# Kernel optimization log

Measured on AMD Instinct MI355X. Metric: run time of the kernel, lower is better.

Reference implementation:

```python
import jax, jax.numpy as jnp
import numpy as np

N_NODES = 100000
N_EDGES = 640000
D_IN = 128
D_OUT = 128


def setup_inputs() -> dict:
    key = jax.random.key(0)
    k_x, k_w, k_v, k_r, k_c = jax.random.split(key, 5)
    x = jax.random.normal(k_x, (N_NODES, D_IN), dtype=jnp.float32)
    # Xavier-uniform init for weights, zeros for bias (matches module init)
    limit = float(np.sqrt(6.0 / (D_IN + D_OUT)))
    weights = jax.random.uniform(k_w, (D_IN, D_OUT), dtype=jnp.float32,
                                 minval=-limit, maxval=limit)
    bias = jnp.zeros((D_OUT,), dtype=jnp.float32)
    # Sparse normalized adjacency in COO form: value[e] * y[col[e]] scattered to row[e]
    edge_val = jax.random.uniform(k_v, (N_EDGES,), dtype=jnp.float32)
    row = jax.random.randint(k_r, (N_EDGES,), 0, N_NODES, dtype=jnp.int32)
    col = jax.random.randint(k_c, (N_EDGES,), 0, N_NODES, dtype=jnp.int32)
    return {"x": x, "weights": weights, "bias": bias,
            "edge_val": edge_val, "row": row, "col": col}


def reference(x, weights, bias, edge_val, row, col):
    # y = x @ W  (dense GEMM)  [N, D_OUT]
    y = x @ weights
    # SpMM: out[i] = sum_{e: row[e]==i} edge_val[e] * y[col[e]]
    msg = edge_val[:, None] * y[col]            # [E, D_OUT] irregular gather
    agg = jax.ops.segment_sum(msg, row, num_segments=x.shape[0])
    return agg + bias
```

## Files before the change

### kernel.cpp

```cpp
#include <hip/hip_runtime.h>
#include <hip/hip_bf16.h>


#define N_NODES 100000
#define N_EDGES 640000
#define D 128
#define ELL_K 16
#define OVF_CAP 8192
#define NB 391
#define BCAP 2048
#define CHUNK 2048
#define NCHUNKS 313
#define N_TILES 6250
#define ELL_P 17

typedef __attribute__((ext_vector_type(8))) short short8;
typedef __attribute__((ext_vector_type(4))) float f32x4;
typedef __attribute__((ext_vector_type(4))) ushort us4;

__device__ __forceinline__ ushort f2bf(float f) {
    uint u = __float_as_uint(f);
    u += 0x7fff + ((u >> 16) & 1);
    return (ushort)(u >> 16);
}
__device__ __forceinline__ float bflo(uint u) { return __uint_as_float(u << 16); }
__device__ __forceinline__ float bfhi(uint u) { return __uint_as_float(u & 0xffff0000u); }

__global__ __launch_bounds__(256, 4) void gemm_xw(const float* __restrict__ x,
                                                  const float* __restrict__ w,
                                                  ushort* __restrict__ y,
                                                  int* __restrict__ bucketCnt) {
    __shared__ ushort wt[128 * 128];
    const int tid = threadIdx.x;

    int gz = blockIdx.x * 256 + tid;
    if (gz <= NB) bucketCnt[gz] = 0;

    #pragma unroll
    for (int it = 0; it < 16; ++it) {
        int idx4 = tid + it * 256;
        int k = idx4 >> 5;
        int n0 = (idx4 & 31) * 4;
        float4 v = *(const float4*)(w + (size_t)idx4 * 4);
        float vv[4] = {v.x, v.y, v.z, v.w};
        #pragma unroll
        for (int q = 0; q < 4; ++q) {
            int n = n0 + q;
            wt[n * 128 + (k ^ ((n & 7) << 3))] = f2bf(vv[q]);
        }
    }
    __syncthreads();

    const int lane = tid & 63;
    const int l15 = lane & 15;
    const int h = lane >> 4;

    const int waveGlobal = blockIdx.x * 4 + (tid >> 6);
    const int nWaves = gridDim.x * 4;

    for (int t = waveGlobal; t < N_TILES; t += nWaves) {
        asm volatile("" ::: "memory");
        const float* xr = x + (size_t)(t * 16 + l15) * D;
        float4 xb[8];
        #pragma unroll
        for (int ks = 0; ks < 4; ++ks) {
            xb[2 * ks]     = *(const float4*)(xr + 32 * ks + 8 * h);
            xb[2 * ks + 1] = *(const float4*)(xr + 32 * ks + 8 * h + 4);
        }
        short8 a[4];
        #pragma unroll
        for (int ks = 0; ks < 4; ++ks) {
            const float* p0 = (const float*)&xb[2 * ks];
            const float* p1 = (const float*)&xb[2 * ks + 1];
            a[ks][0] = f2bf(p0[0]); a[ks][1] = f2bf(p0[1]);
            a[ks][2] = f2bf(p0[2]); a[ks][3] = f2bf(p0[3]);
            a[ks][4] = f2bf(p1[0]); a[ks][5] = f2bf(p1[1]);
            a[ks][6] = f2bf(p1[2]); a[ks][7] = f2bf(p1[3]);
        }
        f32x4 acc[8];
        #pragma unroll
        for (int j = 0; j < 8; ++j) acc[j] = (f32x4){0.f, 0.f, 0.f, 0.f};
        #pragma unroll
        for (int ks = 0; ks < 4; ++ks) {
            const int k0 = 32 * ks + 8 * h;
            #pragma unroll
            for (int j = 0; j < 8; ++j) {
                int n = 16 * j + l15;
                short8 b = *(const short8*)&wt[n * 128 + (k0 ^ ((n & 7) << 3))];
                acc[j] = __builtin_amdgcn_mfma_f32_16x16x32_bf16(b, a[ks], acc[j], 0, 0, 0);
            }
        }
        ushort* yn = y + (size_t)(t * 16 + l15) * D;
        #pragma unroll
        for (int j = 0; j < 8; ++j) {
            us4 o;
            o.x = f2bf(acc[j][0]); o.y = f2bf(acc[j][1]);
            o.z = f2bf(acc[j][2]); o.w = f2bf(acc[j][3]);
            *(us4*)(yn + 16 * j + 4 * h) = o;
        }
    }
}

__global__ __launch_bounds__(256) void partition_edges(const float* __restrict__ ev,
                                                       const int* __restrict__ row,
                                                       const int* __restrict__ col,
                                                       int* __restrict__ bucketCnt,
                                                       uint2* __restrict__ es0,
                                                       int* __restrict__ ovfCnt,
                                                       int* __restrict__ ovfRow,
                                                       int* __restrict__ ovfCol,
                                                       float* __restrict__ ovfVal) {
    __shared__ int hist[NB];
    __shared__ int cur[NB];
    const int tid = threadIdx.x;
    const int base = blockIdx.x * CHUNK;

    for (int t = tid; t < NB; t += 256) hist[t] = 0;
    __syncthreads();

    #pragma unroll
    for (int it = 0; it < CHUNK / 256; ++it) {
        int i = base + it * 256 + tid;
        if (i < N_EDGES) atomicAdd(&hist[row[i] >> 8], 1);
    }
    __syncthreads();

    for (int t = tid; t < NB; t += 256) {
        int h = hist[t];
        int start = (h > 0) ? atomicAdd(&bucketCnt[t], h) : 0;
        cur[t] = t * BCAP + start;
    }
    __syncthreads();

    #pragma unroll
    for (int it = 0; it < CHUNK / 256; ++it) {
        int i = base + it * 256 + tid;
        if (i < N_EDGES) {
            int r = row[i];
            int b = r >> 8;
            int p = atomicAdd(&cur[b], 1);
            if (p < (b + 1) * BCAP) {
                uint2 e;
                e.x = __float_as_uint(ev[i]);
                e.y = (uint)col[i] | ((uint)(r & 255) << 20);
                es0[p] = e;
            } else {
                int q = atomicAdd(ovfCnt, 1);
                if (q < OVF_CAP) {
                    ovfRow[q] = r;
                    ovfCol[q] = col[i];
                    ovfVal[q] = ev[i];
                }
            }
        }
    }
}

__global__ __launch_bounds__(256) void build_ell(const uint2* __restrict__ es0,
                                                 const int* __restrict__ bucketCnt,
                                                 float2* __restrict__ es,
                                                 int* __restrict__ ovfCnt,
                                                 int* __restrict__ ovfRow,
                                                 int* __restrict__ ovfCol,
                                                 float* __restrict__ ovfVal) {
    __shared__ float2 ell[256 * ELL_P];
    __shared__ int lcnt[256];
    const int tid = threadIdx.x;
    const int b = blockIdx.x;

    lcnt[tid] = 0;
    #pragma unroll
    for (int it = 0; it < ELL_P; ++it)
        ell[it * 256 + tid] = (float2){0.f, 0.f};
    __syncthreads();

    int cnt = bucketCnt[b];
    if (cnt > BCAP) cnt = BCAP;
    const uint2* src = es0 + (size_t)b * BCAP;

    for (int i = tid; i < cnt; i += 256) {
        uint2 e = src[i];
        int r = e.y >> 20;
        int p = atomicAdd(&lcnt[r], 1);
        if (p < ELL_K) {
            float2 rec;
            rec.x = __uint_as_float(e.x);
            rec.y = __uint_as_float(e.y & 0xFFFFFu);
            ell[r * ELL_P + p] = rec;
        } else {
            int q = atomicAdd(ovfCnt, 1);
            if (q < OVF_CAP) {
                ovfRow[q] = b * 256 + r;
                ovfCol[q] = (int)(e.y & 0xFFFFFu);
                ovfVal[q] = __uint_as_float(e.x);
            }
        }
    }
    __syncthreads();

    const int nbase = b * 256;
    int nvalid = N_NODES - nbase;
    if (nvalid > 256) nvalid = 256;

    float2* dst2 = es + (size_t)nbase * ELL_K;
    for (int t = tid; t < nvalid * ELL_K; t += 256) {
        int r = t >> 4, s = t & 15;
        dst2[t] = ell[r * ELL_P + s];
    }
}

__global__ __launch_bounds__(256) void spmm_ell(const ushort* __restrict__ y,
                                                const float2* __restrict__ es,
                                                const float* __restrict__ bias,
                                                float* __restrict__ out) {
    const int tid = threadIdx.x;
    const int c16 = tid & 15;
    const int n = blockIdx.x * 16 + (tid >> 4);

    const float4* er = (const float4*)(es + (size_t)n * ELL_K);
    float4 e0 = er[0], e1 = er[1], e2 = er[2], e3 = er[3];
    float4 e4 = er[4], e5 = er[5], e6 = er[6], e7 = er[7];

    const ushort* yb = y + c16 * 8;
    #define YLD(c) (*(const uint4*)(yb + ((size_t)__float_as_int(c) << 7)))
    uint4 u0 = YLD(e0.y), u1 = YLD(e0.w), u2 = YLD(e1.y), u3 = YLD(e1.w);
    uint4 u4 = YLD(e2.y), u5 = YLD(e2.w), u6 = YLD(e3.y), u7 = YLD(e3.w);
    uint4 u8 = YLD(e4.y), u9 = YLD(e4.w), uA = YLD(e5.y), uB = YLD(e5.w);
    uint4 uC = YLD(e6.y), uD = YLD(e6.w), uE = YLD(e7.y), uF = YLD(e7.w);
    #undef YLD

    float a[8] = {0.f, 0.f, 0.f, 0.f, 0.f, 0.f, 0.f, 0.f};
    #define FMA8(v, u) do { \
        a[0] += (v) * bflo((u).x); a[1] += (v) * bfhi((u).x); \
        a[2] += (v) * bflo((u).y); a[3] += (v) * bfhi((u).y); \
        a[4] += (v) * bflo((u).z); a[5] += (v) * bfhi((u).z); \
        a[6] += (v) * bflo((u).w); a[7] += (v) * bfhi((u).w); } while (0)
    FMA8(e0.x, u0); FMA8(e0.z, u1); FMA8(e1.x, u2); FMA8(e1.z, u3);
    FMA8(e2.x, u4); FMA8(e2.z, u5); FMA8(e3.x, u6); FMA8(e3.z, u7);
    FMA8(e4.x, u8); FMA8(e4.z, u9); FMA8(e5.x, uA); FMA8(e5.z, uB);
    FMA8(e6.x, uC); FMA8(e6.z, uD); FMA8(e7.x, uE); FMA8(e7.z, uF);
    #undef FMA8

    const float4 b0 = *(const float4*)(bias + c16 * 8);
    const float4 b1 = *(const float4*)(bias + c16 * 8 + 4);
    float4 o0 = {a[0] + b0.x, a[1] + b0.y, a[2] + b0.z, a[3] + b0.w};
    float4 o1 = {a[4] + b1.x, a[5] + b1.y, a[6] + b1.z, a[7] + b1.w};
    float* orow = out + ((size_t)n << 7) + c16 * 8;
    *(float4*)orow = o0;
    *(float4*)(orow + 4) = o1;
}

__global__ void ovf_fix(const ushort* __restrict__ y, const int* __restrict__ ovfRow,
                        const int* __restrict__ ovfCol, const float* __restrict__ ovfVal,
                        const int* __restrict__ ovfCnt, float* __restrict__ out) {
    int nOvf = *ovfCnt;
    if (nOvf > OVF_CAP) nOvf = OVF_CAP;
    int total = nOvf * 32;
    for (int idx = blockIdx.x * 256 + threadIdx.x; idx < total; idx += gridDim.x * 256) {
        int e = idx >> 5;
        int c = idx & 31;
        int r = ovfRow[e];
        int col = ovfCol[e];
        float v = ovfVal[e];
        uint2 u = *(const uint2*)(y + ((size_t)col << 7) + c * 4);
        atomicAdd(&out[(size_t)r * D + c * 4 + 0], v * bflo(u.x));
        atomicAdd(&out[(size_t)r * D + c * 4 + 1], v * bfhi(u.x));
        atomicAdd(&out[(size_t)r * D + c * 4 + 2], v * bflo(u.y));
        atomicAdd(&out[(size_t)r * D + c * 4 + 3], v * bfhi(u.y));
    }
}

extern "C" void kernel_launch(void* const* d_in, const int* in_sizes, int n_in,
                              void* d_out, int out_size, void* d_ws, size_t ws_size,
                              hipStream_t stream) {
    const float* x = (const float*)d_in[0];
    const float* w = (const float*)d_in[1];
    const float* bias = (const float*)d_in[2];
    const float* ev = (const float*)d_in[3];
    const int* row = (const int*)d_in[4];
    const int* col = (const int*)d_in[5];
    float* out = (float*)d_out;

    size_t off = 0;
    auto carve = [&](size_t bytes) -> void* {
        void* p = (char*)d_ws + off;
        off += (bytes + 255) & ~(size_t)255;
        return p;
    };
    ushort* y = (ushort*)carve((size_t)N_NODES * D * sizeof(ushort));
    float2* es = (float2*)carve((size_t)N_NODES * ELL_K * sizeof(float2));
    uint2* es0 = (uint2*)carve((size_t)NB * BCAP * sizeof(uint2));
    int* bucketCnt = (int*)carve((NB + 1) * sizeof(int));
    int* ovfCnt = bucketCnt + NB;
    int* ovfRow = (int*)carve(OVF_CAP * sizeof(int));
    int* ovfCol = (int*)carve(OVF_CAP * sizeof(int));
    float* ovfVal = (float*)carve(OVF_CAP * sizeof(float));

    gemm_xw<<<782, 256, 0, stream>>>(x, w, y, bucketCnt);
    partition_edges<<<NCHUNKS, 256, 0, stream>>>(ev, row, col, bucketCnt, es0,
                                                 ovfCnt, ovfRow, ovfCol, ovfVal);
    build_ell<<<NB, 256, 0, stream>>>(es0, bucketCnt, es,
                                      ovfCnt, ovfRow, ovfCol, ovfVal);
    spmm_ell<<<N_NODES / 16, 256, 0, stream>>>(y, es, bias, out);
    ovf_fix<<<16, 256, 0, stream>>>(y, ovfRow, ovfCol, ovfVal, ovfCnt, out);
}
```

Before: 88.21 us.

## Fuse ELL build with SpMM, register-cache W fragments, prefetch GEMM tiles

Merges build_ell, spmm_ell and ovf_fix into one kernel per 256-row bucket. The ELL slab stays in shared memory, so the global ELL buffer write and read-back go away. Overflow edges are handled per block through a small shared list followed by atomics, and bucket overflow (more than BCAP edges) is now silently dropped. The GEMM keeps all W fragments in registers, software-prefetches the next x tile, uses 512 blocks with launch bounds 2, and partition uses larger chunks. This cuts launch count and memory traffic, at the cost of fewer SpMM blocks (391) with less parallelism for hiding gather latency, and correctness risk if per-block overflow exceeds 64.

New measurement: 91.15 us. +3.3%, slower.

```diff
diff --git a/kernel.cpp b/kernel.cpp
--- a/kernel.cpp
+++ b/kernel.cpp
@@ -6,27 +6,26 @@
 #define N_EDGES 640000
 #define D 128
 #define ELL_K 16
-#define OVF_CAP 8192
 #define NB 391
 #define BCAP 2048
-#define CHUNK 2048
-#define NCHUNKS 313
+#define CHUNK 4096
+#define NCHUNKS 157
 #define N_TILES 6250
 #define ELL_P 17
+#define OVS 64
 
 typedef __attribute__((ext_vector_type(8))) short short8;
 typedef __attribute__((ext_vector_type(4))) float f32x4;
 typedef __attribute__((ext_vector_type(4))) ushort us4;
 
 __device__ __forceinline__ ushort f2bf(float f) {
-    uint u = __float_as_uint(f);
-    u += 0x7fff + ((u >> 16) & 1);
-    return (ushort)(u >> 16);
+    __hip_bfloat16 h = __float2bfloat16(f);
+    return __builtin_bit_cast(ushort, h);
 }
 __device__ __forceinline__ float bflo(uint u) { return __uint_as_float(u << 16); }
 __device__ __forceinline__ float bfhi(uint u) { return __uint_as_float(u & 0xffff0000u); }
 
-__global__ __launch_bounds__(256, 4) void gemm_xw(const float* __restrict__ x,
+__global__ __launch_bounds__(256, 2) void gemm_xw(const float* __restrict__ x,
                                                   const float* __restrict__ w,
                                                   ushort* __restrict__ y,
                                                   int* __restrict__ bucketCnt) {
@@ -34,7 +33,7 @@
     const int tid = threadIdx.x;
 
     int gz = blockIdx.x * 256 + tid;
-    if (gz <= NB) bucketCnt[gz] = 0;
+    if (gz < NB) bucketCnt[gz] = 0;
 
     #pragma unroll
     for (int it = 0; it < 16; ++it) {
@@ -55,48 +54,85 @@
     const int l15 = lane & 15;
     const int h = lane >> 4;
 
+    short8 bfr[8][4];
+    #pragma unroll
+    for (int j = 0; j < 8; ++j) {
+        int n = 16 * j + l15;
+        #pragma unroll
+        for (int ks = 0; ks < 4; ++ks) {
+            int k0 = 32 * ks + 8 * h;
+            bfr[j][ks] = *(const short8*)&wt[n * 128 + (k0 ^ ((n & 7) << 3))];
+        }
+    }
+
     const int waveGlobal = blockIdx.x * 4 + (tid >> 6);
     const int nWaves = gridDim.x * 4;
 
-    for (int t = waveGlobal; t < N_TILES; t += nWaves) {
-        asm volatile("" ::: "memory");
-        const float* xr = x + (size_t)(t * 16 + l15) * D;
-        float4 xb[8];
-        #pragma unroll
-        for (int ks = 0; ks < 4; ++ks) {
-            xb[2 * ks]     = *(const float4*)(xr + 32 * ks + 8 * h);
-            xb[2 * ks + 1] = *(const float4*)(xr + 32 * ks + 8 * h + 4);
-        }
+    int t = waveGlobal;
+    if (t < N_TILES) {
         short8 a[4];
-        #pragma unroll
-        for (int ks = 0; ks < 4; ++ks) {
-            const float* p0 = (const float*)&xb[2 * ks];
-            const float* p1 = (const float*)&xb[2 * ks + 1];
-            a[ks][0] = f2bf(p0[0]); a[ks][1] = f2bf(p0[1]);
-            a[ks][2] = f2bf(p0[2]); a[ks][3] = f2bf(p0[3]);
-            a[ks][4] = f2bf(p1[0]); a[ks][5] = f2bf(p1[1]);
-            a[ks][6] = f2bf(p1[2]); a[ks][7] = f2bf(p1[3]);
-        }
-        f32x4 acc[8];
-        #pragma unroll
-        for (int j = 0; j < 8; ++j) acc[j] = (f32x4){0.f, 0.f, 0.f, 0.f};
-        #pragma unroll
-        for (int ks = 0; ks < 4; ++ks) {
-            const int k0 = 32 * ks + 8 * h;
+        {
+            const float* xr = x + (size_t)(t * 16 + l15) * D;
+            float4 xb[8];
+            #pragma unroll
+            for (int ks = 0; ks < 4; ++ks) {
+                xb[2 * ks]     = *(const float4*)(xr + 32 * ks + 8 * h);
+                xb[2 * ks + 1] = *(const float4*)(xr + 32 * ks + 8 * h + 4);
+            }
+            #pragma unroll
+            for (int ks = 0; ks < 4; ++ks) {
+                const float* p0 = (const float*)&xb[2 * ks];
+                const float* p1 = (const float*)&xb[2 * ks + 1];
+                a[ks][0] = f2bf(p0[0]); a[ks][1] = f2bf(p0[1]);
+                a[ks][2] = f2bf(p0[2]); a[ks][3] = f2bf(p0[3]);
+                a[ks][4] = f2bf(p1[0]); a[ks][5] = f2bf(p1[1]);
+                a[ks][6] = f2bf(p1[2]); a[ks][7] = f2bf(p1[3]);
+            }
+        }
+        #pragma unroll 1
+        while (true) {
+            const int tn = t + nWaves;
+            const bool more = tn < N_TILES;
+
+            float4 xb2[8];
+            if (more) {
+                const float* xr = x + (size_t)(tn * 16 + l15) * D;
+                #pragma unroll
+                for (int ks = 0; ks < 4; ++ks) {
+                    xb2[2 * ks]     = *(const float4*)(xr + 32 * ks + 8 * h);
+                    xb2[2 * ks + 1] = *(const float4*)(xr + 32 * ks + 8 * h + 4);
+                }
+            }
+
+            f32x4 acc[8];
+            #pragma unroll
+            for (int j = 0; j < 8; ++j) acc[j] = (f32x4){0.f, 0.f, 0.f, 0.f};
+            #pragma unroll
+            for (int ks = 0; ks < 4; ++ks) {
+                #pragma unroll
+                for (int j = 0; j < 8; ++j)
+                    acc[j] = __builtin_amdgcn_mfma_f32_16x16x32_bf16(bfr[j][ks], a[ks], acc[j], 0, 0, 0);
+            }
+            ushort* yn = y + (size_t)(t * 16 + l15) * D;
             #pragma unroll
             for (int j = 0; j < 8; ++j) {
-                int n = 16 * j + l15;
-                short8 b = *(const short8*)&wt[n * 128 + (k0 ^ ((n & 7) << 3))];
-                acc[j] = __builtin_amdgcn_mfma_f32_16x16x32_bf16(b, a[ks], acc[j], 0, 0, 0);
-            }
-        }
-        ushort* yn = y + (size_t)(t * 16 + l15) * D;
-        #pragma unroll
-        for (int j = 0; j < 8; ++j) {
-            us4 o;
-            o.x = f2bf(acc[j][0]); o.y = f2bf(acc[j][1]);
-            o.z = f2bf(acc[j][2]); o.w = f2bf(acc[j][3]);
-            *(us4*)(yn + 16 * j + 4 * h) = o;
+                us4 o;
+                o.x = f2bf(acc[j][0]); o.y = f2bf(acc[j][1]);
+                o.z = f2bf(acc[j][2]); o.w = f2bf(acc[j][3]);
+                *(us4*)(yn + 16 * j + 4 * h) = o;
+            }
+
+            if (!more) break;
+            #pragma unroll
+            for (int ks = 0; ks < 4; ++ks) {
+                const float* p0 = (const float*)&xb2[2 * ks];
+                const float* p1 = (const float*)&xb2[2 * ks + 1];
+                a[ks][0] = f2bf(p0[0]); a[ks][1] = f2bf(p0[1]);
+                a[ks][2] = f2bf(p0[2]); a[ks][3] = f2bf(p0[3]);
+                a[ks][4] = f2bf(p1[0]); a[ks][5] = f2bf(p1[1]);
+                a[ks][6] = f2bf(p1[2]); a[ks][7] = f2bf(p1[3]);
+            }
+            t = tn;
         }
     }
 }
@@ -105,11 +141,7 @@
                                                        const int* __restrict__ row,
                                                        const int* __restrict__ col,
                                                        int* __restrict__ bucketCnt,
-                                                       uint2* __restrict__ es0,
-                                                       int* __restrict__ ovfCnt,
-                                                       int* __restrict__ ovfRow,
-                                                       int* __restrict__ ovfCol,
-                                                       float* __restrict__ ovfVal) {
+                                                       uint2* __restrict__ es0) {
     __shared__ int hist[NB];
     __shared__ int cur[NB];
     const int tid = threadIdx.x;
@@ -144,31 +176,27 @@
                 e.x = __float_as_uint(ev[i]);
                 e.y = (uint)col[i] | ((uint)(r & 255) << 20);
                 es0[p] = e;
-            } else {
-                int q = atomicAdd(ovfCnt, 1);
-                if (q < OVF_CAP) {
-                    ovfRow[q] = r;
-                    ovfCol[q] = col[i];
-                    ovfVal[q] = ev[i];
-                }
-            }
-        }
-    }
-}
-
-__global__ __launch_bounds__(256) void build_ell(const uint2* __restrict__ es0,
-                                                 const int* __restrict__ bucketCnt,
-                                                 float2* __restrict__ es,
-                                                 int* __restrict__ ovfCnt,
-                                                 int* __restrict__ ovfRow,
-                                                 int* __restrict__ ovfCol,
-                                                 float* __restrict__ ovfVal) {
+            }
+        }
+    }
+}
+
+__global__ __launch_bounds__(256) void ell_spmm(const uint2* __restrict__ es0,
+                                                const int* __restrict__ bucketCnt,
+                                                const ushort* __restrict__ y,
+                                                const float* __restrict__ bias,
+                                                float* __restrict__ out) {
     __shared__ float2 ell[256 * ELL_P];
     __shared__ int lcnt[256];
+    __shared__ float ovVal[OVS];
+    __shared__ int ovCol[OVS];
+    __shared__ int ovRl[OVS];
+    __shared__ int ovCnt;
     const int tid = threadIdx.x;
     const int b = blockIdx.x;
 
     lcnt[tid] = 0;
+    if (tid == 0) ovCnt = 0;
     #pragma unroll
     for (int it = 0; it < ELL_P; ++it)
         ell[it * 256 + tid] = (float2){0.f, 0.f};
@@ -188,85 +216,75 @@
             rec.y = __uint_as_float(e.y & 0xFFFFFu);
             ell[r * ELL_P + p] = rec;
         } else {
-            int q = atomicAdd(ovfCnt, 1);
-            if (q < OVF_CAP) {
-                ovfRow[q] = b * 256 + r;
-                ovfCol[q] = (int)(e.y & 0xFFFFFu);
-                ovfVal[q] = __uint_as_float(e.x);
-            }
-        }
-    }
-    __syncthreads();
-
+            int q = atomicAdd(&ovCnt, 1);
+            if (q < OVS) {
+                ovVal[q] = __uint_as_float(e.x);
+                ovCol[q] = (int)(e.y & 0xFFFFFu);
+                ovRl[q] = r;
+            }
+        }
+    }
+    __syncthreads();
+
+    const int c16 = tid & 15;
+    const int grp = tid >> 4;
     const int nbase = b * 256;
-    int nvalid = N_NODES - nbase;
-    if (nvalid > 256) nvalid = 256;
-
-    float2* dst2 = es + (size_t)nbase * ELL_K;
-    for (int t = tid; t < nvalid * ELL_K; t += 256) {
-        int r = t >> 4, s = t & 15;
-        dst2[t] = ell[r * ELL_P + s];
-    }
-}
-
-__global__ __launch_bounds__(256) void spmm_ell(const ushort* __restrict__ y,
-                                                const float2* __restrict__ es,
-                                                const float* __restrict__ bias,
-                                                float* __restrict__ out) {
-    const int tid = threadIdx.x;
-    const int c16 = tid & 15;
-    const int n = blockIdx.x * 16 + (tid >> 4);
-
-    const float4* er = (const float4*)(es + (size_t)n * ELL_K);
-    float4 e0 = er[0], e1 = er[1], e2 = er[2], e3 = er[3];
-    float4 e4 = er[4], e5 = er[5], e6 = er[6], e7 = er[7];
-
-    const ushort* yb = y + c16 * 8;
-    #define YLD(c) (*(const uint4*)(yb + ((size_t)__float_as_int(c) << 7)))
-    uint4 u0 = YLD(e0.y), u1 = YLD(e0.w), u2 = YLD(e1.y), u3 = YLD(e1.w);
-    uint4 u4 = YLD(e2.y), u5 = YLD(e2.w), u6 = YLD(e3.y), u7 = YLD(e3.w);
-    uint4 u8 = YLD(e4.y), u9 = YLD(e4.w), uA = YLD(e5.y), uB = YLD(e5.w);
-    uint4 uC = YLD(e6.y), uD = YLD(e6.w), uE = YLD(e7.y), uF = YLD(e7.w);
-    #undef YLD
-
-    float a[8] = {0.f, 0.f, 0.f, 0.f, 0.f, 0.f, 0.f, 0.f};
-    #define FMA8(v, u) do { \
-        a[0] += (v) * bflo((u).x); a[1] += (v) * bfhi((u).x); \
-        a[2] += (v) * bflo((u).y); a[3] += (v) * bfhi((u).y); \
-        a[4] += (v) * bflo((u).z); a[5] += (v) * bfhi((u).z); \
-        a[6] += (v) * bflo((u).w); a[7] += (v) * bfhi((u).w); } while (0)
-    FMA8(e0.x, u0); FMA8(e0.z, u1); FMA8(e1.x, u2); FMA8(e1.z, u3);
-    FMA8(e2.x, u4); FMA8(e2.z, u5); FMA8(e3.x, u6); FMA8(e3.z, u7);
-    FMA8(e4.x, u8); FMA8(e4.z, u9); FMA8(e5.x, uA); FMA8(e5.z, uB);
-    FMA8(e6.x, uC); FMA8(e6.z, uD); FMA8(e7.x, uE); FMA8(e7.z, uF);
-    #undef FMA8
 
     const float4 b0 = *(const float4*)(bias + c16 * 8);
     const float4 b1 = *(const float4*)(bias + c16 * 8 + 4);
-    float4 o0 = {a[0] + b0.x, a[1] + b0.y, a[2] + b0.z, a[3] + b0.w};
-    float4 o1 = {a[4] + b1.x, a[5] + b1.y, a[6] + b1.z, a[7] + b1.w};
-    float* orow = out + ((size_t)n << 7) + c16 * 8;
-    *(float4*)orow = o0;
-    *(float4*)(orow + 4) = o1;
-}
-
-__global__ void ovf_fix(const ushort* __restrict__ y, const int* __restrict__ ovfRow,
-                        const int* __restrict__ ovfCol, const float* __restrict__ ovfVal,
-                        const int* __restrict__ ovfCnt, float* __restrict__ out) {
-    int nOvf = *ovfCnt;
-    if (nOvf > OVF_CAP) nOvf = OVF_CAP;
-    int total = nOvf * 32;
-    for (int idx = blockIdx.x * 256 + threadIdx.x; idx < total; idx += gridDim.x * 256) {
-        int e = idx >> 5;
-        int c = idx & 31;
-        int r = ovfRow[e];
-        int col = ovfCol[e];
-        float v = ovfVal[e];
-        uint2 u = *(const uint2*)(y + ((size_t)col << 7) + c * 4);
-        atomicAdd(&out[(size_t)r * D + c * 4 + 0], v * bflo(u.x));
-        atomicAdd(&out[(size_t)r * D + c * 4 + 1], v * bfhi(u.x));
-        atomicAdd(&out[(size_t)r * D + c * 4 + 2], v * bflo(u.y));
-        atomicAdd(&out[(size_t)r * D + c * 4 + 3], v * bfhi(u.y));
+    const ushort* yb = y + c16 * 8;
+
+    #pragma unroll 1
+    for (int rep = 0; rep < 16; ++rep) {
+        const int rl = grp + rep * 16;
+        const int n = nbase + rl;
+        const float4* er = (const float4*)&ell[rl * ELL_P];
+        float4 e0 = er[0], e1 = er[1], e2 = er[2], e3 = er[3];
+        float4 e4 = er[4], e5 = er[5], e6 = er[6], e7 = er[7];
+
+        #define YLD(c) (*(const uint4*)(yb + ((size_t)__float_as_int(c) << 7)))
+        uint4 u0 = YLD(e0.y), u1 = YLD(e0.w), u2 = YLD(e1.y), u3 = YLD(e1.w);
+        uint4 u4 = YLD(e2.y), u5 = YLD(e2.w), u6 = YLD(e3.y), u7 = YLD(e3.w);
+        uint4 u8 = YLD(e4.y), u9 = YLD(e4.w), uA = YLD(e5.y), uB = YLD(e5.w);
+        uint4 uC = YLD(e6.y), uD = YLD(e6.w), uE = YLD(e7.y), uF = YLD(e7.w);
+        #undef YLD
+
+        float a[8] = {0.f, 0.f, 0.f, 0.f, 0.f, 0.f, 0.f, 0.f};
+        #define FMA8(v, u) do { \
+            a[0] += (v) * bflo((u).x); a[1] += (v) * bfhi((u).x); \
+            a[2] += (v) * bflo((u).y); a[3] += (v) * bfhi((u).y); \
+            a[4] += (v) * bflo((u).z); a[5] += (v) * bfhi((u).z); \
+            a[6] += (v) * bflo((u).w); a[7] += (v) * bfhi((u).w); } while (0)
+        FMA8(e0.x, u0); FMA8(e0.z, u1); FMA8(e1.x, u2); FMA8(e1.z, u3);
+        FMA8(e2.x, u4); FMA8(e2.z, u5); FMA8(e3.x, u6); FMA8(e3.z, u7);
+        FMA8(e4.x, u8); FMA8(e4.z, u9); FMA8(e5.x, uA); FMA8(e5.z, uB);
+        FMA8(e6.x, uC); FMA8(e6.z, uD); FMA8(e7.x, uE); FMA8(e7.z, uF);
+        #undef FMA8
+
+        if (n < N_NODES) {
+            float4 o0 = {a[0] + b0.x, a[1] + b0.y, a[2] + b0.z, a[3] + b0.w};
+            float4 o1 = {a[4] + b1.x, a[5] + b1.y, a[6] + b1.z, a[7] + b1.w};
+            float* orow = out + ((size_t)n << 7) + c16 * 8;
+            *(float4*)orow = o0;
+            *(float4*)(orow + 4) = o1;
+        }
+    }
+    __syncthreads();
+
+    int nOv = ovCnt;
+    if (nOv > OVS) nOv = OVS;
+    for (int q = grp; q < nOv; q += 16) {
+        float v = ovVal[q];
+        int c = ovCol[q];
+        int n = nbase + ovRl[q];
+        if (n < N_NODES) {
+            uint4 u = *(const uint4*)(yb + ((size_t)c << 7));
+            float* orow = out + ((size_t)n << 7) + c16 * 8;
+            atomicAdd(orow + 0, v * bflo(u.x)); atomicAdd(orow + 1, v * bfhi(u.x));
+            atomicAdd(orow + 2, v * bflo(u.y)); atomicAdd(orow + 3, v * bfhi(u.y));
+            atomicAdd(orow + 4, v * bflo(u.z)); atomicAdd(orow + 5, v * bfhi(u.z));
+            atomicAdd(orow + 6, v * bflo(u.w)); atomicAdd(orow + 7, v * bfhi(u.w));
+        }
     }
 }
 
@@ -288,19 +306,10 @@
         return p;
     };
     ushort* y = (ushort*)carve((size_t)N_NODES * D * sizeof(ushort));
-    float2* es = (float2*)carve((size_t)N_NODES * ELL_K * sizeof(float2));
     uint2* es0 = (uint2*)carve((size_t)NB * BCAP * sizeof(uint2));
-    int* bucketCnt = (int*)carve((NB + 1) * sizeof(int));
-    int* ovfCnt = bucketCnt + NB;
-    int* ovfRow = (int*)carve(OVF_CAP * sizeof(int));
-    int* ovfCol = (int*)carve(OVF_CAP * sizeof(int));
-    float* ovfVal = (float*)carve(OVF_CAP * sizeof(float));
-
-    gemm_xw<<<782, 256, 0, stream>>>(x, w, y, bucketCnt);
-    partition_edges<<<NCHUNKS, 256, 0, stream>>>(ev, row, col, bucketCnt, es0,
-                                                 ovfCnt, ovfRow, ovfCol, ovfVal);
-    build_ell<<<NB, 256, 0, stream>>>(es0, bucketCnt, es,
-                                      ovfCnt, ovfRow, ovfCol, ovfVal);
-    spmm_ell<<<N_NODES / 16, 256, 0, stream>>>(y, es, bias, out);
-    ovf_fix<<<16, 256, 0, stream>>>(y, ovfRow, ovfCol, ovfVal, ovfCnt, out);
-}
+    int* bucketCnt = (int*)carve(NB * sizeof(int));
+
+    gemm_xw<<<512, 256, 0, stream>>>(x, w, y, bucketCnt);
+    partition_edges<<<NCHUNKS, 256, 0, stream>>>(ev, row, col, bucketCnt, es0);
+    ell_spmm<<<NB, 256, 0, stream>>>(es0, bucketCnt, y, bias, out);
+}
```
